# Performance work log

Hardware: AMD Instinct MI355X
Metric: run time of the kernel (lower is better)

The kernel has to match this reference:

```python
import jax, jax.numpy as jnp
import numpy as np

N_NODES = 8192
N_EDGES = 262144
D_IN, D_HID, D_OUT = 128, 64, 32
DROP_P = 0.1


def _glorot(key, shape):
    lim = (6.0 / (shape[0] + shape[1])) ** 0.5
    return jax.random.uniform(key, shape, jnp.float32, -lim, lim)


def setup_inputs() -> dict:
    key = jax.random.key(0)
    ks = jax.random.split(key, 8)
    x = jax.random.normal(ks[0], (N_NODES, D_IN), jnp.float32)
    edge_index = jax.random.randint(ks[1], (2, N_EDGES), 0, N_NODES, jnp.int64)
    # GCNConv params: linear weight [in, out] (x @ W) + bias, 3 layers
    W0 = _glorot(ks[2], (D_IN, D_HID)); b0 = jnp.zeros((D_HID,), jnp.float32)
    W1 = _glorot(ks[3], (D_HID, D_HID)); b1 = jnp.zeros((D_HID,), jnp.float32)
    W2 = _glorot(ks[4], (D_HID, D_OUT)); b2 = jnp.zeros((D_OUT,), jnp.float32)
    return {"x": x, "W0": W0, "b0": b0, "W1": W1, "b1": b1,
            "W2": W2, "b2": b2, "edge_index": edge_index}


def _gcn(adj, x, W, b):
    # PyG GCNConv: add self-loops, symmetric normalization D^-1/2 (A+I) D^-1/2
    n = adj.shape[0]
    a = adj + jnp.eye(n, dtype=adj.dtype)
    dinv = jax.lax.rsqrt(a.sum(axis=1))  # deg >= 1 due to self-loop
    a = dinv[:, None] * a * dinv[None, :]
    return a @ (x @ W) + b


def reference(x, W0, b0, W1, b1, W2, b2, edge_index):
    n = x.shape[0]
    # binary dense adjacency of the ORIGINAL graph (to_dense_adj analogue)
    adj0 = jnp.zeros((n, n), x.dtype).at[edge_index[0], edge_index[1]].set(1.0)
    rng = jax.random.key(42)
    params = [(W0, b0), (W1, b1), (W2, b2)]
    adj = adj0
    z = x
    for i, (W, b) in enumerate(params):
        z = jax.nn.relu(_gcn(adj, z, W, b))
        kd, kb = jax.random.split(jax.random.fold_in(rng, i))
        keep = jax.random.bernoulli(kd, 1.0 - DROP_P, z.shape)
        z = jnp.where(keep, z / (1.0 - DROP_P), 0.0)  # Dropout(0.1), train mode
        if i < len(params) - 1:  # last resample never affects the output
            prob = jax.nn.sigmoid(z @ z.T)                      # [N, N]
            sample = (jax.random.uniform(kb, prob.shape) < prob).astype(z.dtype)
            adj = adj0 * sample  # Bernoulli-masked original edges
    return z
```

## Files before the change

kernel.cpp:

```cpp
#include <hip/hip_runtime.h>
#include <stdint.h>
#include <math.h>

#define NN 8192
#define NE 262144
#define WPR 256
#define CAP 96

struct TFKey { uint32_t a, b; };

__host__ __device__ static inline void tf2x32(uint32_t k0, uint32_t k1,
                                              uint32_t x0, uint32_t x1,
                                              uint32_t* o0, uint32_t* o1) {
  uint32_t ks2 = k0 ^ k1 ^ 0x1BD11BDAu;
#define TF_ROT(x, r) (((x) << (r)) | ((x) >> (32 - (r))))
#define TF_R(r) { x0 += x1; x1 = TF_ROT(x1, r); x1 ^= x0; }
  x0 += k0; x1 += k1;
  TF_R(13) TF_R(15) TF_R(26) TF_R(6)
  x0 += k1;  x1 += ks2 + 1u;
  TF_R(17) TF_R(29) TF_R(16) TF_R(24)
  x0 += ks2; x1 += k0 + 2u;
  TF_R(13) TF_R(15) TF_R(26) TF_R(6)
  x0 += k0;  x1 += k1 + 3u;
  TF_R(17) TF_R(29) TF_R(16) TF_R(24)
  x0 += k1;  x1 += ks2 + 4u;
  TF_R(13) TF_R(15) TF_R(26) TF_R(6)
  x0 += ks2; x1 += k0 + 5u;
  *o0 = x0; *o1 = x1;
#undef TF_R
#undef TF_ROT
}

__device__ static inline float tf_uniform(TFKey k, uint32_t n) {
  uint32_t o0, o1;
  tf2x32(k.a, k.b, 0u, n, &o0, &o1);
  uint32_t bits = o0 ^ o1;
  return __uint_as_float((bits >> 9) | 0x3f800000u) - 1.0f;
}

__global__ __launch_bounds__(256) void k_init(const int* __restrict__ e,
                                              uint32_t* __restrict__ dense,
                                              uint32_t* __restrict__ deg,
                                              uint32_t* __restrict__ flag) {
  uint32_t t = blockIdx.x * 256 + threadIdx.x;
  ((uint4*)dense)[t] = make_uint4(0u, 0u, 0u, 0u);
  if (t < NN) deg[t] = 0u;
  if (blockIdx.x == 0) {
    const unsigned long long* p = (const unsigned long long*)e;
    bool bad = false;
    for (int q = 0; q < 8; ++q)
      bad |= (p[threadIdx.x * 8 + q] >= 8192ull);
    __shared__ uint32_t sh[4];
    unsigned long long b = __ballot(bad);
    if ((threadIdx.x & 63) == 0) sh[threadIdx.x >> 6] = (b != 0ull) ? 1u : 0u;
    __syncthreads();
    if (threadIdx.x == 0) flag[0] = sh[0] | sh[1] | sh[2] | sh[3];
  }
}

__global__ __launch_bounds__(256) void k_build(const int* __restrict__ e,
                                               const uint32_t* __restrict__ flag,
                                               uint32_t* __restrict__ dense,
                                               uint32_t* __restrict__ deg,
                                               uint16_t* __restrict__ cols) {
  int ed = blockIdx.x * 256 + threadIdx.x;
  int r, c;
  if (*flag) { r = e[ed]; c = e[ed + NE]; }
  else { const long long* p = (const long long*)e; r = (int)p[ed]; c = (int)p[ed + NE]; }
  uint32_t bit = 1u << (c & 31);
  uint32_t old = atomicOr(&dense[(size_t)r * WPR + (c >> 5)], bit);
  if (!(old & bit)) {
    uint32_t s = atomicAdd(&deg[r], 1u);
    if (s < CAP) cols[(size_t)r * CAP + s] = (uint16_t)c;
  }
}

template<int K, int N, bool DINV0>
__global__ __launch_bounds__(256) void k_dg(const float* __restrict__ A,
                                            const float* __restrict__ Wb,
                                            float* __restrict__ H,
                                            const uint32_t* __restrict__ deg,
                                            float* __restrict__ dinv) {
  constexpr int GB = NN * N / 256;
  if (blockIdx.x < GB) {
    int t = blockIdx.x * 256 + threadIdx.x;
    int i = t / N, c = t % N;
    double a0 = 0.0, a1 = 0.0;
#pragma unroll 8
    for (int k = 0; k < K; k += 2) {
      a0 += (double)A[(size_t)i * K + k] * (double)Wb[(size_t)k * N + c];
      a1 += (double)A[(size_t)i * K + k + 1] * (double)Wb[(size_t)(k + 1) * N + c];
    }
    H[t] = (float)(a0 + a1);
  } else if (DINV0) {
    int i = (blockIdx.x - GB) * 256 + threadIdx.x;
    dinv[i] = (float)(1.0 / sqrt((double)(deg[i] + 1u)));
  }
}

template<int D>
__global__ __launch_bounds__(256) void k_agg(const uint16_t* __restrict__ cols,
                                             const uint32_t* __restrict__ deg,
                                             const uint8_t* __restrict__ mask,
                                             const float* __restrict__ h,
                                             const float* __restrict__ dinv,
                                             const float* __restrict__ bias,
                                             TFKey kd, float* __restrict__ zout) {
  int lane = threadIdx.x & 63;
  int i = blockIdx.x * 4 + (threadIdx.x >> 6);
  bool act = lane < D;
  float di = dinv[i];
  uint32_t du = deg[i];
  uint32_t d = du < (uint32_t)CAP ? du : (uint32_t)CAP;
  const uint16_t* cr = cols + (size_t)i * CAP;
  const uint8_t* mr = mask ? mask + (size_t)i * CAP : (const uint8_t*)nullptr;
  double a0 = 0.0, a1 = 0.0;
  uint32_t s = 0;
  for (; s + 1 < d; s += 2) {
    int j0 = cr[s], j1 = cr[s + 1];
    bool m0 = !mr || mr[s], m1 = !mr || mr[s + 1];
    if (act) {
      if (m0) { float c0 = di * dinv[j0]; a0 += (double)c0 * (double)h[(size_t)j0 * D + lane]; }
      if (m1) { float c1 = di * dinv[j1]; a1 += (double)c1 * (double)h[(size_t)j1 * D + lane]; }
    }
  }
  if (s < d && (!mr || mr[s]) && act) {
    int j = cr[s];
    float c = di * dinv[j];
    a0 += (double)c * (double)h[(size_t)j * D + lane];
  }
  if (act) {
    double acc = a0 + a1;
    float cI = di * di;
    acc += (double)cI * (double)h[(size_t)i * D + lane];
    float sv = (float)acc;
    float pre = fmaxf(sv + bias[lane], 0.0f);
    float u = tf_uniform(kd, (uint32_t)(i * D + lane));
    zout[(size_t)i * D + lane] = (u < 0.9f) ? (pre / 0.9f) : 0.0f;
  }
}

__global__ __launch_bounds__(256) void k_sample(const uint16_t* __restrict__ cols,
                                                const uint32_t* __restrict__ deg,
                                                const float* __restrict__ z,
                                                TFKey kb,
                                                uint8_t* __restrict__ mask,
                                                float* __restrict__ dinv) {
  int lane = threadIdx.x & 63;
  int i = blockIdx.x * 4 + (threadIdx.x >> 6);
  int g = lane >> 4, l = lane & 15;
  float4 zi = *(const float4*)(z + (size_t)i * 64 + 4 * l);
  uint32_t du = deg[i];
  uint32_t d = du < (uint32_t)CAP ? du : (uint32_t)CAP;
  const uint16_t* cr = cols + (size_t)i * CAP;
  uint8_t* mr = mask + (size_t)i * CAP;
  int cnt = 0;
  for (uint32_t base = 0; base < d; base += 4) {
    uint32_t s = base + (uint32_t)g;
    bool on = s < d;
    int j = 0;
    if (on) j = cr[s];
    float4 b = *(const float4*)(z + (size_t)j * 64 + 4 * l);
    double p = (double)zi.x * (double)b.x + (double)zi.y * (double)b.y
             + (double)zi.z * (double)b.z + (double)zi.w * (double)b.w;
    p += __shfl_xor(p, 1, 64);
    p += __shfl_xor(p, 2, 64);
    p += __shfl_xor(p, 4, 64);
    p += __shfl_xor(p, 8, 64);
    if (l == 0 && on) {
      float dot32 = (float)p;
      float prob = (float)(1.0 / (1.0 + exp(-(double)dot32)));
      float u = tf_uniform(kb, (uint32_t)((i << 13) | j));
      uint8_t m = (u < prob) ? 1u : 0u;
      mr[s] = m;
      cnt += m;
    }
  }
  cnt += __shfl_xor(cnt, 16, 64);
  cnt += __shfl_xor(cnt, 32, 64);
  if (lane == 0) dinv[i] = (float)(1.0 / sqrt((double)(cnt + 1)));
}

extern "C" void kernel_launch(void* const* d_in, const int* in_sizes, int n_in,
                              void* d_out, int out_size, void* d_ws, size_t ws_size,
                              hipStream_t stream) {
  (void)in_sizes; (void)n_in; (void)out_size; (void)ws_size;
  const float* x  = (const float*)d_in[0];
  const float* W0 = (const float*)d_in[1];
  const float* b0 = (const float*)d_in[2];
  const float* W1 = (const float*)d_in[3];
  const float* b1 = (const float*)d_in[4];
  const float* W2 = (const float*)d_in[5];
  const float* b2 = (const float*)d_in[6];
  const int* ei = (const int*)d_in[7];
  float* out = (float*)d_out;

  uint8_t* base = (uint8_t*)d_ws;
  uint32_t* dense = (uint32_t*)(base);
  float* h        = (float*)(base);
  float* z        = (float*)(base + 2097152);
  uint32_t* deg   = (uint32_t*)(base + 8388608);
  uint16_t* cols  = (uint16_t*)(base + 8388608 + 32768);
  uint8_t*  mask  = (uint8_t*)(base + 8388608 + 32768 + 1572864);
  float*    dinv  = (float*)(base + 8388608 + 32768 + 1572864 + 786432);
  uint32_t* flag  = (uint32_t*)(base + 8388608 + 32768 + 1572864 + 786432 + 32768);

  TFKey kd[3], kb[3];
  for (uint32_t i = 0; i < 3; ++i) {
    uint32_t la, lb;
    tf2x32(0u, 42u, 0u, i, &la, &lb);
    tf2x32(la, lb, 0u, 0u, &kd[i].a, &kd[i].b);
    tf2x32(la, lb, 0u, 1u, &kb[i].a, &kb[i].b);
  }

  k_init <<<NN * WPR / (4 * 256), 256, 0, stream>>>(ei, dense, deg, flag);
  k_build<<<NE / 256, 256, 0, stream>>>(ei, flag, dense, deg, cols);

  k_dg<128, 64, true><<<NN * 64 / 256 + NN / 256, 256, 0, stream>>>(x, W0, h, deg, dinv);
  k_agg<64><<<NN / 4, 256, 0, stream>>>(cols, deg, nullptr, h, dinv, b0, kd[0], z);
  k_sample<<<NN / 4, 256, 0, stream>>>(cols, deg, z, kb[0], mask, dinv);

  k_dg<64, 64, false><<<NN * 64 / 256, 256, 0, stream>>>(z, W1, h, deg, dinv);
  k_agg<64><<<NN / 4, 256, 0, stream>>>(cols, deg, mask, h, dinv, b1, kd[1], z);
  k_sample<<<NN / 4, 256, 0, stream>>>(cols, deg, z, kb[1], mask, dinv);

  k_dg<64, 32, false><<<NN * 32 / 256, 256, 0, stream>>>(z, W2, h, deg, dinv);
  k_agg<32><<<NN / 4, 256, 0, stream>>>(cols, deg, mask, h, dinv, b2, kd[2], out);
}
```

Baseline: 238.4 us.

## Fuse all GCN stages into one persistent cooperative kernel with grid syncs

Replaces the chain of ten separate kernel launches with a single cooperative kernel. It walks through the init, build, GEMM, aggregate and sample phases using grid-stride loops, with grid.sync() between dependent phases. The sample phase and the next GEMM now share one phase because they touch independent buffers, which removes one barrier per layer. The aim is to cut per-launch overhead and kernel-boundary drain. In exchange it adds grid-wide barrier costs and limits occupancy to the number of co-resident blocks, and it falls back to the old launch path if cooperative launch is unsupported.

```diff
diff --git a/kernel.cpp b/kernel.cpp
--- a/kernel.cpp
+++ b/kernel.cpp
@@ -1,6 +1,9 @@
 #include <hip/hip_runtime.h>
+#include <hip/hip_cooperative_groups.h>
 #include <stdint.h>
 #include <math.h>
+
+namespace cg = cooperative_groups;
 
 #define NN 8192
 #define NE 262144
@@ -38,6 +41,179 @@
   return __uint_as_float((bits >> 9) | 0x3f800000u) - 1.0f;
 }
 
+
+struct Params {
+  const float* x; const float* W0; const float* b0;
+  const float* W1; const float* b1; const float* W2; const float* b2;
+  const int* ei; float* out;
+  uint32_t* dense; float* h; float* z;
+  uint32_t* deg; uint16_t* cols; uint8_t* mask; float* dinv; uint32_t* flag;
+  TFKey kd0, kb0, kd1, kb1, kd2;
+};
+
+template<int K, int N>
+__device__ __forceinline__ void gemm_ph(const float* __restrict__ A,
+                                        const float* __restrict__ Wb,
+                                        float* __restrict__ H, int tid, int tot) {
+  for (int t = tid; t < NN * N; t += tot) {
+    int i = t / N, c = t % N;
+    double a0 = 0.0, a1 = 0.0;
+#pragma unroll 8
+    for (int k = 0; k < K; k += 2) {
+      a0 += (double)A[(size_t)i * K + k] * (double)Wb[(size_t)k * N + c];
+      a1 += (double)A[(size_t)i * K + k + 1] * (double)Wb[(size_t)(k + 1) * N + c];
+    }
+    H[t] = (float)(a0 + a1);
+  }
+}
+
+template<int D>
+__device__ __forceinline__ void agg_ph(const uint16_t* __restrict__ cols,
+                                       const uint32_t* __restrict__ deg,
+                                       const uint8_t* __restrict__ mask,
+                                       const float* __restrict__ h,
+                                       const float* __restrict__ dinv,
+                                       const float* __restrict__ bias,
+                                       TFKey kd, float* __restrict__ zout,
+                                       int wid, int nw, int lane) {
+  bool act = lane < D;
+  for (int i = wid; i < NN; i += nw) {
+    float di = dinv[i];
+    uint32_t du = deg[i];
+    uint32_t d = du < (uint32_t)CAP ? du : (uint32_t)CAP;
+    const uint16_t* cr = cols + (size_t)i * CAP;
+    const uint8_t* mr = mask ? mask + (size_t)i * CAP : (const uint8_t*)nullptr;
+    double a0 = 0.0, a1 = 0.0;
+    uint32_t s = 0;
+    for (; s + 1 < d; s += 2) {
+      int j0 = cr[s], j1 = cr[s + 1];
+      bool m0 = !mr || mr[s], m1 = !mr || mr[s + 1];
+      if (act) {
+        if (m0) { float c0 = di * dinv[j0]; a0 += (double)c0 * (double)h[(size_t)j0 * D + lane]; }
+        if (m1) { float c1 = di * dinv[j1]; a1 += (double)c1 * (double)h[(size_t)j1 * D + lane]; }
+      }
+    }
+    if (s < d && (!mr || mr[s]) && act) {
+      int j = cr[s];
+      float c = di * dinv[j];
+      a0 += (double)c * (double)h[(size_t)j * D + lane];
+    }
+    if (act) {
+      double acc = a0 + a1;
+      float cI = di * di;
+      acc += (double)cI * (double)h[(size_t)i * D + lane];
+      float sv = (float)acc;
+      float pre = fmaxf(sv + bias[lane], 0.0f);
+      float u = tf_uniform(kd, (uint32_t)(i * D + lane));
+      zout[(size_t)i * D + lane] = (u < 0.9f) ? (pre / 0.9f) : 0.0f;
+    }
+  }
+}
+
+__device__ __forceinline__ void sample_ph(const uint16_t* __restrict__ cols,
+                                          const uint32_t* __restrict__ deg,
+                                          const float* __restrict__ z,
+                                          TFKey kb, uint8_t* __restrict__ mask,
+                                          float* __restrict__ dinv,
+                                          int wid, int nw, int lane) {
+  int g = lane >> 4, l = lane & 15;
+  for (int i = wid; i < NN; i += nw) {
+    float4 zi = *(const float4*)(z + (size_t)i * 64 + 4 * l);
+    uint32_t du = deg[i];
+    uint32_t d = du < (uint32_t)CAP ? du : (uint32_t)CAP;
+    const uint16_t* cr = cols + (size_t)i * CAP;
+    uint8_t* mr = mask + (size_t)i * CAP;
+    int cnt = 0;
+    for (uint32_t base = 0; base < d; base += 4) {
+      uint32_t s = base + (uint32_t)g;
+      bool on = s < d;
+      int j = 0;
+      if (on) j = cr[s];
+      float4 b = *(const float4*)(z + (size_t)j * 64 + 4 * l);
+      double p = (double)zi.x * (double)b.x + (double)zi.y * (double)b.y
+               + (double)zi.z * (double)b.z + (double)zi.w * (double)b.w;
+      p += __shfl_xor(p, 1, 64);
+      p += __shfl_xor(p, 2, 64);
+      p += __shfl_xor(p, 4, 64);
+      p += __shfl_xor(p, 8, 64);
+      if (l == 0 && on) {
+        float dot32 = (float)p;
+        float prob = (float)(1.0 / (1.0 + exp(-(double)dot32)));
+        float u = tf_uniform(kb, (uint32_t)((i << 13) | j));
+        uint8_t m = (u < prob) ? 1u : 0u;
+        mr[s] = m;
+        cnt += m;
+      }
+    }
+    cnt += __shfl_xor(cnt, 16, 64);
+    cnt += __shfl_xor(cnt, 32, 64);
+    if (lane == 0) dinv[i] = (float)(1.0 / sqrt((double)(cnt + 1)));
+  }
+}
+
+__global__ __launch_bounds__(256, 4) void fused(Params p) {
+  cg::grid_group grid = cg::this_grid();
+  const int tid = blockIdx.x * 256 + threadIdx.x;
+  const int tot = gridDim.x * 256;
+  const int lane = threadIdx.x & 63;
+  const int wid = tid >> 6;
+  const int nw = tot >> 6;
+
+  for (int t = tid; t < NN * WPR / 4; t += tot)
+    ((uint4*)p.dense)[t] = make_uint4(0u, 0u, 0u, 0u);
+  for (int t = tid; t < NN; t += tot) p.deg[t] = 0u;
+  if (blockIdx.x == 0) {
+    const unsigned long long* q = (const unsigned long long*)p.ei;
+    bool bad = false;
+    for (int k = 0; k < 8; ++k)
+      bad |= (q[threadIdx.x * 8 + k] >= 8192ull);
+    __shared__ uint32_t sh[4];
+    unsigned long long b = __ballot(bad);
+    if ((threadIdx.x & 63) == 0) sh[threadIdx.x >> 6] = (b != 0ull) ? 1u : 0u;
+    __syncthreads();
+    if (threadIdx.x == 0) p.flag[0] = sh[0] | sh[1] | sh[2] | sh[3];
+  }
+  grid.sync();
+
+  {
+    const uint32_t isI32 = *p.flag;
+    for (int ed = tid; ed < NE; ed += tot) {
+      int r, c;
+      if (isI32) { r = p.ei[ed]; c = p.ei[ed + NE]; }
+      else { const long long* q = (const long long*)p.ei; r = (int)q[ed]; c = (int)q[ed + NE]; }
+      uint32_t bit = 1u << (c & 31);
+      uint32_t old = atomicOr(&p.dense[(size_t)r * WPR + (c >> 5)], bit);
+      if (!(old & bit)) {
+        uint32_t s = atomicAdd(&p.deg[r], 1u);
+        if (s < CAP) p.cols[(size_t)r * CAP + s] = (uint16_t)c;
+      }
+    }
+  }
+  grid.sync();
+
+  gemm_ph<128, 64>(p.x, p.W0, p.h, tid, tot);
+  for (int t = tid; t < NN; t += tot)
+    p.dinv[t] = (float)(1.0 / sqrt((double)(p.deg[t] + 1u)));
+  grid.sync();
+
+  agg_ph<64>(p.cols, p.deg, nullptr, p.h, p.dinv, p.b0, p.kd0, p.z, wid, nw, lane);
+  grid.sync();
+
+  sample_ph(p.cols, p.deg, p.z, p.kb0, p.mask, p.dinv, wid, nw, lane);
+  gemm_ph<64, 64>(p.z, p.W1, p.h, tid, tot);
+  grid.sync();
+
+  agg_ph<64>(p.cols, p.deg, p.mask, p.h, p.dinv, p.b1, p.kd1, p.z, wid, nw, lane);
+  grid.sync();
+
+  sample_ph(p.cols, p.deg, p.z, p.kb1, p.mask, p.dinv, wid, nw, lane);
+  gemm_ph<64, 32>(p.z, p.W2, p.h, tid, tot);
+  grid.sync();
+
+  agg_ph<32>(p.cols, p.deg, p.mask, p.h, p.dinv, p.b2, p.kd2, p.out, wid, nw, lane);
+}
+
+
 __global__ __launch_bounds__(256) void k_init(const int* __restrict__ e,
                                               uint32_t* __restrict__ dense,
                                               uint32_t* __restrict__ deg,
@@ -48,8 +224,7 @@
   if (blockIdx.x == 0) {
     const unsigned long long* p = (const unsigned long long*)e;
     bool bad = false;
-    for (int q = 0; q < 8; ++q)
-      bad |= (p[threadIdx.x * 8 + q] >= 8192ull);
+    for (int q = 0; q < 8; ++q) bad |= (p[threadIdx.x * 8 + q] >= 8192ull);
     __shared__ uint32_t sh[4];
     unsigned long long b = __ballot(bad);
     if ((threadIdx.x & 63) == 0) sh[threadIdx.x >> 6] = (b != 0ull) ? 1u : 0u;
@@ -84,14 +259,7 @@
   constexpr int GB = NN * N / 256;
   if (blockIdx.x < GB) {
     int t = blockIdx.x * 256 + threadIdx.x;
-    int i = t / N, c = t % N;
-    double a0 = 0.0, a1 = 0.0;
-#pragma unroll 8
-    for (int k = 0; k < K; k += 2) {
-      a0 += (double)A[(size_t)i * K + k] * (double)Wb[(size_t)k * N + c];
-      a1 += (double)A[(size_t)i * K + k + 1] * (double)Wb[(size_t)(k + 1) * N + c];
-    }
-    H[t] = (float)(a0 + a1);
+    gemm_ph<K, N>(A, Wb, H, t, NN * N);
   } else if (DINV0) {
     int i = (blockIdx.x - GB) * 256 + threadIdx.x;
     dinv[i] = (float)(1.0 / sqrt((double)(deg[i] + 1u)));
@@ -107,37 +275,8 @@
                                              const float* __restrict__ bias,
                                              TFKey kd, float* __restrict__ zout) {
   int lane = threadIdx.x & 63;
-  int i = blockIdx.x * 4 + (threadIdx.x >> 6);
-  bool act = lane < D;
-  float di = dinv[i];
-  uint32_t du = deg[i];
-  uint32_t d = du < (uint32_t)CAP ? du : (uint32_t)CAP;
-  const uint16_t* cr = cols + (size_t)i * CAP;
-  const uint8_t* mr = mask ? mask + (size_t)i * CAP : (const uint8_t*)nullptr;
-  double a0 = 0.0, a1 = 0.0;
-  uint32_t s = 0;
-  for (; s + 1 < d; s += 2) {
-    int j0 = cr[s], j1 = cr[s + 1];
-    bool m0 = !mr || mr[s], m1 = !mr || mr[s + 1];
-    if (act) {
-      if (m0) { float c0 = di * dinv[j0]; a0 += (double)c0 * (double)h[(size_t)j0 * D + lane]; }
-      if (m1) { float c1 = di * dinv[j1]; a1 += (double)c1 * (double)h[(size_t)j1 * D + lane]; }
-    }
-  }
-  if (s < d && (!mr || mr[s]) && act) {
-    int j = cr[s];
-    float c = di * dinv[j];
-    a0 += (double)c * (double)h[(size_t)j * D + lane];
-  }
-  if (act) {
-    double acc = a0 + a1;
-    float cI = di * di;
-    acc += (double)cI * (double)h[(size_t)i * D + lane];
-    float sv = (float)acc;
-    float pre = fmaxf(sv + bias[lane], 0.0f);
-    float u = tf_uniform(kd, (uint32_t)(i * D + lane));
-    zout[(size_t)i * D + lane] = (u < 0.9f) ? (pre / 0.9f) : 0.0f;
-  }
+  int wid = blockIdx.x * 4 + (threadIdx.x >> 6);
+  agg_ph<D>(cols, deg, mask, h, dinv, bias, kd, zout, wid, NN, lane);
 }
 
 __global__ __launch_bounds__(256) void k_sample(const uint16_t* __restrict__ cols,
@@ -147,39 +286,10 @@
                                                 uint8_t* __restrict__ mask,
                                                 float* __restrict__ dinv) {
   int lane = threadIdx.x & 63;
-  int i = blockIdx.x * 4 + (threadIdx.x >> 6);
-  int g = lane >> 4, l = lane & 15;
-  float4 zi = *(const float4*)(z + (size_t)i * 64 + 4 * l);
-  uint32_t du = deg[i];
-  uint32_t d = du < (uint32_t)CAP ? du : (uint32_t)CAP;
-  const uint16_t* cr = cols + (size_t)i * CAP;
-  uint8_t* mr = mask + (size_t)i * CAP;
-  int cnt = 0;
-  for (uint32_t base = 0; base < d; base += 4) {
-    uint32_t s = base + (uint32_t)g;
-    bool on = s < d;
-    int j = 0;
-    if (on) j = cr[s];
-    float4 b = *(const float4*)(z + (size_t)j * 64 + 4 * l);
-    double p = (double)zi.x * (double)b.x + (double)zi.y * (double)b.y
-             + (double)zi.z * (double)b.z + (double)zi.w * (double)b.w;
-    p += __shfl_xor(p, 1, 64);
-    p += __shfl_xor(p, 2, 64);
-    p += __shfl_xor(p, 4, 64);
-    p += __shfl_xor(p, 8, 64);
-    if (l == 0 && on) {
-      float dot32 = (float)p;
-      float prob = (float)(1.0 / (1.0 + exp(-(double)dot32)));
-      float u = tf_uniform(kb, (uint32_t)((i << 13) | j));
-      uint8_t m = (u < prob) ? 1u : 0u;
-      mr[s] = m;
-      cnt += m;
-    }
-  }
-  cnt += __shfl_xor(cnt, 16, 64);
-  cnt += __shfl_xor(cnt, 32, 64);
-  if (lane == 0) dinv[i] = (float)(1.0 / sqrt((double)(cnt + 1)));
-}
+  int wid = blockIdx.x * 4 + (threadIdx.x >> 6);
+  sample_ph(cols, deg, z, kb, mask, dinv, wid, NN, lane);
+}
+
 
 extern "C" void kernel_launch(void* const* d_in, const int* in_sizes, int n_in,
                               void* d_out, int out_size, void* d_ws, size_t ws_size,
@@ -213,17 +323,46 @@
     tf2x32(la, lb, 0u, 1u, &kb[i].a, &kb[i].b);
   }
 
+  static int coop = -1;
+  static int nblk = 0;
+  if (coop < 0) {
+    int dev = 0; (void)hipGetDevice(&dev);
+    int attr = 0;
+    if (hipDeviceGetAttribute(&attr, hipDeviceAttributeCooperativeLaunch, dev) != hipSuccess)
+      attr = 0;
+    coop = attr;
+    if (coop) {
+      int per = 0;
+      if (hipOccupancyMaxActiveBlocksPerMultiprocessor(
+              &per, reinterpret_cast<const void*>(fused), 256, 0) != hipSuccess || per < 1)
+        per = 1;
+      int cus = 0;
+      if (hipDeviceGetAttribute(&cus, hipDeviceAttributeMultiprocessorCount, dev) != hipSuccess || cus < 1)
+        cus = 256;
+      nblk = per * cus;
+      if (nblk > 2048) nblk = 2048;
+      if (nblk < 1) nblk = 1;
+    }
+  }
+
+  if (coop) {
+    Params p = { x, W0, b0, W1, b1, W2, b2, ei, out,
+                 dense, h, z, deg, cols, mask, dinv, flag,
+                 kd[0], kb[0], kd[1], kb[1], kd[2] };
+    void* args[] = { &p };
+    (void)hipLaunchCooperativeKernel(reinterpret_cast<const void*>(fused),
+                                     dim3(nblk), dim3(256), args, 0, stream);
+    return;
+  }
+
   k_init <<<NN * WPR / (4 * 256), 256, 0, stream>>>(ei, dense, deg, flag);
   k_build<<<NE / 256, 256, 0, stream>>>(ei, flag, dense, deg, cols);
-
   k_dg<128, 64, true><<<NN * 64 / 256 + NN / 256, 256, 0, stream>>>(x, W0, h, deg, dinv);
   k_agg<64><<<NN / 4, 256, 0, stream>>>(cols, deg, nullptr, h, dinv, b0, kd[0], z);
   k_sample<<<NN / 4, 256, 0, stream>>>(cols, deg, z, kb[0], mask, dinv);
-
   k_dg<64, 64, false><<<NN * 64 / 256, 256, 0, stream>>>(z, W1, h, deg, dinv);
   k_agg<64><<<NN / 4, 256, 0, stream>>>(cols, deg, mask, h, dinv, b1, kd[1], z);
   k_sample<<<NN / 4, 256, 0, stream>>>(cols, deg, z, kb[1], mask, dinv);
-
   k_dg<64, 32, false><<<NN * 32 / 256, 256, 0, stream>>>(z, W2, h, deg, dinv);
   k_agg<32><<<NN / 4, 256, 0, stream>>>(cols, deg, mask, h, dinv, b2, kd[2], out);
 }
```

New measurement: 917.9 us. +285.0%, slower.

## Replace dense bitmap dedup with per-row shared-memory dedup and fuse GEMM with sampling

Applied to the files above, without the earlier changes.

Drops the 8MB dense adjacency bitmap and its zero-fill. Edges are now appended to per-row column lists with raw duplicates, then deduplicated per row in a shared-memory bitmap kernel that also computes degree and dinv. The first GEMM is merged with edge insertion, and each layer's sampling kernel is merged with the next layer's feature GEMM, cutting launches and letting independent work overlap. Risk: with duplicates counted toward CAP before dedup, rows with many duplicate edges could overflow the 96-entry cap, and the order of neighbour lists becomes nondeterministic.

```diff
diff --git a/kernel.cpp b/kernel.cpp
--- a/kernel.cpp
+++ b/kernel.cpp
@@ -4,7 +4,6 @@
 
 #define NN 8192
 #define NE 262144
-#define WPR 256
 #define CAP 96
 
 struct TFKey { uint32_t a, b; };
@@ -38,76 +37,30 @@
   return __uint_as_float((bits >> 9) | 0x3f800000u) - 1.0f;
 }
 
-__global__ __launch_bounds__(256) void k_init(const int* __restrict__ e,
-                                              uint32_t* __restrict__ dense,
-                                              uint32_t* __restrict__ deg,
-                                              uint32_t* __restrict__ flag) {
-  uint32_t t = blockIdx.x * 256 + threadIdx.x;
-  ((uint4*)dense)[t] = make_uint4(0u, 0u, 0u, 0u);
-  if (t < NN) deg[t] = 0u;
-  if (blockIdx.x == 0) {
-    const unsigned long long* p = (const unsigned long long*)e;
-    bool bad = false;
-    for (int q = 0; q < 8; ++q)
-      bad |= (p[threadIdx.x * 8 + q] >= 8192ull);
-    __shared__ uint32_t sh[4];
-    unsigned long long b = __ballot(bad);
-    if ((threadIdx.x & 63) == 0) sh[threadIdx.x >> 6] = (b != 0ull) ? 1u : 0u;
-    __syncthreads();
-    if (threadIdx.x == 0) flag[0] = sh[0] | sh[1] | sh[2] | sh[3];
-  }
-}
-
-__global__ __launch_bounds__(256) void k_build(const int* __restrict__ e,
-                                               const uint32_t* __restrict__ flag,
-                                               uint32_t* __restrict__ dense,
-                                               uint32_t* __restrict__ deg,
-                                               uint16_t* __restrict__ cols) {
-  int ed = blockIdx.x * 256 + threadIdx.x;
-  int r, c;
-  if (*flag) { r = e[ed]; c = e[ed + NE]; }
-  else { const long long* p = (const long long*)e; r = (int)p[ed]; c = (int)p[ed + NE]; }
-  uint32_t bit = 1u << (c & 31);
-  uint32_t old = atomicOr(&dense[(size_t)r * WPR + (c >> 5)], bit);
-  if (!(old & bit)) {
-    uint32_t s = atomicAdd(&deg[r], 1u);
-    if (s < CAP) cols[(size_t)r * CAP + s] = (uint16_t)c;
-  }
-}
-
-template<int K, int N, bool DINV0>
-__global__ __launch_bounds__(256) void k_dg(const float* __restrict__ A,
-                                            const float* __restrict__ Wb,
-                                            float* __restrict__ H,
-                                            const uint32_t* __restrict__ deg,
-                                            float* __restrict__ dinv) {
-  constexpr int GB = NN * N / 256;
-  if (blockIdx.x < GB) {
-    int t = blockIdx.x * 256 + threadIdx.x;
-    int i = t / N, c = t % N;
-    double a0 = 0.0, a1 = 0.0;
+
+template<int K, int N>
+__device__ __forceinline__ void gemm_elem(const float* __restrict__ A,
+                                          const float* __restrict__ Wb,
+                                          float* __restrict__ H, int t) {
+  int i = t / N, c = t % N;
+  double a0 = 0.0, a1 = 0.0;
 #pragma unroll 8
-    for (int k = 0; k < K; k += 2) {
-      a0 += (double)A[(size_t)i * K + k] * (double)Wb[(size_t)k * N + c];
-      a1 += (double)A[(size_t)i * K + k + 1] * (double)Wb[(size_t)(k + 1) * N + c];
-    }
-    H[t] = (float)(a0 + a1);
-  } else if (DINV0) {
-    int i = (blockIdx.x - GB) * 256 + threadIdx.x;
-    dinv[i] = (float)(1.0 / sqrt((double)(deg[i] + 1u)));
-  }
+  for (int k = 0; k < K; k += 2) {
+    a0 += (double)A[(size_t)i * K + k] * (double)Wb[(size_t)k * N + c];
+    a1 += (double)A[(size_t)i * K + k + 1] * (double)Wb[(size_t)(k + 1) * N + c];
+  }
+  H[t] = (float)(a0 + a1);
 }
 
 template<int D>
-__global__ __launch_bounds__(256) void k_agg(const uint16_t* __restrict__ cols,
-                                             const uint32_t* __restrict__ deg,
-                                             const uint8_t* __restrict__ mask,
-                                             const float* __restrict__ h,
-                                             const float* __restrict__ dinv,
-                                             const float* __restrict__ bias,
-                                             TFKey kd, float* __restrict__ zout) {
-  int lane = threadIdx.x & 63;
-  int i = blockIdx.x * 4 + (threadIdx.x >> 6);
+__device__ __forceinline__ void agg_row(const uint16_t* __restrict__ cols,
+                                        const uint32_t* __restrict__ deg,
+                                        const uint8_t* __restrict__ mask,
+                                        const float* __restrict__ h,
+                                        const float* __restrict__ dinv,
+                                        const float* __restrict__ bias,
+                                        TFKey kd, float* __restrict__ zout,
+                                        int i, int lane) {
   bool act = lane < D;
   float di = dinv[i];
   uint32_t du = deg[i];
@@ -140,14 +93,12 @@
   }
 }
 
-__global__ __launch_bounds__(256) void k_sample(const uint16_t* __restrict__ cols,
-                                                const uint32_t* __restrict__ deg,
-                                                const float* __restrict__ z,
-                                                TFKey kb,
-                                                uint8_t* __restrict__ mask,
-                                                float* __restrict__ dinv) {
-  int lane = threadIdx.x & 63;
-  int i = blockIdx.x * 4 + (threadIdx.x >> 6);
+__device__ __forceinline__ void sample_row(const uint16_t* __restrict__ cols,
+                                           const uint32_t* __restrict__ deg,
+                                           const float* __restrict__ z,
+                                           TFKey kb, uint8_t* __restrict__ mask,
+                                           float* __restrict__ dinv,
+                                           int i, int lane) {
   int g = lane >> 4, l = lane & 15;
   float4 zi = *(const float4*)(z + (size_t)i * 64 + 4 * l);
   uint32_t du = deg[i];
@@ -181,6 +132,112 @@
   if (lane == 0) dinv[i] = (float)(1.0 / sqrt((double)(cnt + 1)));
 }
 
+
+__global__ __launch_bounds__(256) void k_init0(const int* __restrict__ e,
+                                               uint32_t* __restrict__ deg,
+                                               uint32_t* __restrict__ flag) {
+  uint32_t t = blockIdx.x * 256 + threadIdx.x;
+  deg[t] = 0u;
+  if (blockIdx.x == 0) {
+    const unsigned long long* p = (const unsigned long long*)e;
+    bool bad = false;
+    for (int q = 0; q < 8; ++q)
+      bad |= (p[threadIdx.x * 8 + q] >= 8192ull);
+    __shared__ uint32_t sh[4];
+    unsigned long long b = __ballot(bad);
+    if ((threadIdx.x & 63) == 0) sh[threadIdx.x >> 6] = (b != 0ull) ? 1u : 0u;
+    __syncthreads();
+    if (threadIdx.x == 0) flag[0] = sh[0] | sh[1] | sh[2] | sh[3];
+  }
+}
+
+__global__ __launch_bounds__(256) void k_g0s(const float* __restrict__ x,
+                                             const float* __restrict__ W0,
+                                             float* __restrict__ h,
+                                             const int* __restrict__ e,
+                                             const uint32_t* __restrict__ flag,
+                                             uint32_t* __restrict__ deg,
+                                             uint16_t* __restrict__ cols) {
+  constexpr int GB0 = NN * 64 / 256;
+  if (blockIdx.x < GB0) {
+    gemm_elem<128, 64>(x, W0, h, blockIdx.x * 256 + threadIdx.x);
+  } else {
+    int ed = (blockIdx.x - GB0) * 256 + threadIdx.x;
+    int r, c;
+    if (*flag) { r = e[ed]; c = e[ed + NE]; }
+    else { const long long* p = (const long long*)e; r = (int)p[ed]; c = (int)p[ed + NE]; }
+    uint32_t s = atomicAdd(&deg[r], 1u);
+    if (s < CAP) cols[(size_t)r * CAP + s] = (uint16_t)c;
+  }
+}
+
+__global__ __launch_bounds__(256) void k_dedup(uint16_t* __restrict__ cols,
+                                               uint32_t* __restrict__ deg,
+                                               float* __restrict__ dinv) {
+  __shared__ uint32_t bits[4][256];
+  __shared__ uint32_t ucnt[4];
+  int lane = threadIdx.x & 63;
+  int wv = threadIdx.x >> 6;
+  int i = blockIdx.x * 4 + wv;
+  ((uint4*)bits[wv])[lane] = make_uint4(0u, 0u, 0u, 0u);
+  if (lane == 0) ucnt[wv] = 0u;
+  __syncthreads();
+  uint32_t draw = deg[i];
+  if (draw > (uint32_t)CAP) draw = (uint32_t)CAP;
+  uint16_t* cr = cols + (size_t)i * CAP;
+  uint32_t c0 = 0xFFFFFFFFu, c1 = 0xFFFFFFFFu;
+  if ((uint32_t)lane < draw) c0 = cr[lane];
+  if ((uint32_t)(lane + 64) < draw) c1 = cr[lane + 64];
+  if (c0 != 0xFFFFFFFFu) {
+    uint32_t bit = 1u << (c0 & 31);
+    uint32_t old = atomicOr(&bits[wv][c0 >> 5], bit);
+    if (!(old & bit)) { uint32_t p = atomicAdd(&ucnt[wv], 1u); cr[p] = (uint16_t)c0; }
+  }
+  if (c1 != 0xFFFFFFFFu) {
+    uint32_t bit = 1u << (c1 & 31);
+    uint32_t old = atomicOr(&bits[wv][c1 >> 5], bit);
+    if (!(old & bit)) { uint32_t p = atomicAdd(&ucnt[wv], 1u); cr[p] = (uint16_t)c1; }
+  }
+  if (lane == 0) {
+    uint32_t u = ucnt[wv];
+    deg[i] = u;
+    dinv[i] = (float)(1.0 / sqrt((double)(u + 1u)));
+  }
+}
+
+template<int D>
+__global__ __launch_bounds__(256) void k_agg(const uint16_t* __restrict__ cols,
+                                             const uint32_t* __restrict__ deg,
+                                             const uint8_t* __restrict__ mask,
+                                             const float* __restrict__ h,
+                                             const float* __restrict__ dinv,
+                                             const float* __restrict__ bias,
+                                             TFKey kd, float* __restrict__ zout) {
+  int lane = threadIdx.x & 63;
+  int i = blockIdx.x * 4 + (threadIdx.x >> 6);
+  agg_row<D>(cols, deg, mask, h, dinv, bias, kd, zout, i, lane);
+}
+
+template<int K, int N>
+__global__ __launch_bounds__(256) void k_sg(const float* __restrict__ z,
+                                            const float* __restrict__ Wb,
+                                            float* __restrict__ h,
+                                            const uint16_t* __restrict__ cols,
+                                            const uint32_t* __restrict__ deg,
+                                            TFKey kb,
+                                            uint8_t* __restrict__ mask,
+                                            float* __restrict__ dinv) {
+  constexpr int GB = NN * N / 256;
+  if (blockIdx.x < GB) {
+    gemm_elem<K, N>(z, Wb, h, blockIdx.x * 256 + threadIdx.x);
+  } else {
+    int lane = threadIdx.x & 63;
+    int i = (blockIdx.x - GB) * 4 + (threadIdx.x >> 6);
+    sample_row(cols, deg, z, kb, mask, dinv, i, lane);
+  }
+}
+
+
 extern "C" void kernel_launch(void* const* d_in, const int* in_sizes, int n_in,
                               void* d_out, int out_size, void* d_ws, size_t ws_size,
                               hipStream_t stream) {
@@ -196,14 +253,13 @@
   float* out = (float*)d_out;
 
   uint8_t* base = (uint8_t*)d_ws;
-  uint32_t* dense = (uint32_t*)(base);
   float* h        = (float*)(base);
   float* z        = (float*)(base + 2097152);
-  uint32_t* deg   = (uint32_t*)(base + 8388608);
-  uint16_t* cols  = (uint16_t*)(base + 8388608 + 32768);
-  uint8_t*  mask  = (uint8_t*)(base + 8388608 + 32768 + 1572864);
-  float*    dinv  = (float*)(base + 8388608 + 32768 + 1572864 + 786432);
-  uint32_t* flag  = (uint32_t*)(base + 8388608 + 32768 + 1572864 + 786432 + 32768);
+  uint32_t* deg   = (uint32_t*)(base + 4194304);
+  uint16_t* cols  = (uint16_t*)(base + 4194304 + 32768);
+  uint8_t*  mask  = (uint8_t*)(base + 4194304 + 32768 + 1572864);
+  float*    dinv  = (float*)(base + 4194304 + 32768 + 1572864 + 786432);
+  uint32_t* flag  = (uint32_t*)(base + 4194304 + 32768 + 1572864 + 786432 + 32768);
 
   TFKey kd[3], kb[3];
   for (uint32_t i = 0; i < 3; ++i) {
@@ -213,17 +269,12 @@
     tf2x32(la, lb, 0u, 1u, &kb[i].a, &kb[i].b);
   }
 
-  k_init <<<NN * WPR / (4 * 256), 256, 0, stream>>>(ei, dense, deg, flag);
-  k_build<<<NE / 256, 256, 0, stream>>>(ei, flag, dense, deg, cols);
-
-  k_dg<128, 64, true><<<NN * 64 / 256 + NN / 256, 256, 0, stream>>>(x, W0, h, deg, dinv);
+  k_init0<<<NN / 256, 256, 0, stream>>>(ei, deg, flag);
+  k_g0s  <<<NN * 64 / 256 + NE / 256, 256, 0, stream>>>(x, W0, h, ei, flag, deg, cols);
+  k_dedup<<<NN / 4, 256, 0, stream>>>(cols, deg, dinv);
   k_agg<64><<<NN / 4, 256, 0, stream>>>(cols, deg, nullptr, h, dinv, b0, kd[0], z);
-  k_sample<<<NN / 4, 256, 0, stream>>>(cols, deg, z, kb[0], mask, dinv);
-
-  k_dg<64, 64, false><<<NN * 64 / 256, 256, 0, stream>>>(z, W1, h, deg, dinv);
+  k_sg<64, 64><<<NN * 64 / 256 + NN / 4, 256, 0, stream>>>(z, W1, h, cols, deg, kb[0], mask, dinv);
   k_agg<64><<<NN / 4, 256, 0, stream>>>(cols, deg, mask, h, dinv, b1, kd[1], z);
-  k_sample<<<NN / 4, 256, 0, stream>>>(cols, deg, z, kb[1], mask, dinv);
-
-  k_dg<64, 32, false><<<NN * 32 / 256, 256, 0, stream>>>(z, W2, h, deg, dinv);
+  k_sg<64, 32><<<NN * 32 / 256 + NN / 4, 256, 0, stream>>>(z, W2, h, cols, deg, kb[1], mask, dinv);
   k_agg<32><<<NN / 4, 256, 0, stream>>>(cols, deg, mask, h, dinv, b2, kd[2], out);
 }
```

After: 219.4 us. -8.0%, faster.
